# Kernel tuning notes

Measured on AMD Instinct MI355X. Metric: run time of the kernel, lower is better.

Reference implementation:

```python
import jax, jax.numpy as jnp
import numpy as np

# Grid constants from voxel_size=(0.2,0.2,4), point_cloud_range=(0,-40,-3,70.4,40,1)
VX, VY, VZ = 0.2, 0.2, 4.0
PCR = (0.0, -40.0, -3.0, 70.4, 40.0, 1.0)
NX, NY, NZ = 352, 400, 1   # round((hi-lo)/v) per axis
BATCH = 2
N_POINTS = 400000
CANVAS = BATCH * NZ * NY * NX  # dense canvas of all voxels (segment ids)
EPS = 1e-3  # BN1d eps from norm_cfg


def _vidx(coors):
    # linear voxel index: b*Z*Y*X + z*Y*X + y*X + x  (coors = [b,z,y,x])
    c = coors.astype(jnp.int32)
    return ((c[:, 0] * NZ + c[:, 1]) * NY + c[:, 2]) * NX + c[:, 3]


def _seg_mean(x, idx):
    # scatter-mean over voxels (DynamicScatter, average_points=True)
    s = jax.ops.segment_sum(x, idx, num_segments=CANVAS)
    c = jax.ops.segment_sum(jnp.ones((x.shape[0], 1), x.dtype), idx, num_segments=CANVAS)
    return s / jnp.maximum(c, 1.0)


def _seg_max(x, idx):
    # scatter-max over voxels (DynamicScatter, average_points=False); empty voxels -> 0
    m = jax.ops.segment_max(x, idx, num_segments=CANVAS)
    c = jax.ops.segment_sum(jnp.ones((x.shape[0],), x.dtype), idx, num_segments=CANVAS)
    return jnp.where((c > 0)[:, None], m, jnp.zeros_like(m))


def _bn_relu(x, g, b):
    # BN1d in training mode (batch stats, biased var), affine, then ReLU
    mu = x.mean(axis=0)
    var = x.var(axis=0)
    return jax.nn.relu((x - mu) * jax.lax.rsqrt(var + EPS) * g + b)


def setup_inputs() -> dict:
    key = jax.random.key(0)
    ks = jax.random.split(key, 6)
    features = jax.random.normal(ks[0], (N_POINTS, 4), jnp.float32)
    # coors [b, z, y, x]; batch column sorted so coors[-1,0]+1 == batch_size
    half = N_POINTS // 2
    b = jnp.concatenate([jnp.zeros(half, jnp.int32), jnp.ones(N_POINTS - half, jnp.int32)])
    z = jnp.zeros(N_POINTS, jnp.int32)  # NZ == 1
    y = jax.random.randint(ks[1], (N_POINTS,), 0, NY, jnp.int32)
    x = jax.random.randint(ks[2], (N_POINTS,), 0, NX, jnp.int32)
    coors = jnp.stack([b, z, y, x], axis=1)
    # VFE params: layer0 Linear(10->64, no bias), layer1 Linear(128->128, no bias)
    W0 = jax.random.normal(ks[3], (10, 64), jnp.float32) * 0.1
    g0 = jnp.ones((64,), jnp.float32)
    b0 = jnp.zeros((64,), jnp.float32)
    W1 = jax.random.normal(ks[4], (128, 128), jnp.float32) * 0.1
    g1 = jnp.ones((128,), jnp.float32)
    b1 = jnp.zeros((128,), jnp.float32)
    return {"features": features, "coors": coors, "W0": W0, "g0": g0, "b0": b0,
            "W1": W1, "g1": g1, "b1": b1}


def reference(features, coors, W0, g0, b0, W1, g1, b1):
    idx = _vidx(coors)
    # cluster center: scatter-mean of point features, gather back to points
    vmean = _seg_mean(features, idx)
    pts_mean = vmean[idx]
    f_cluster = features[:, :3] - pts_mean[:, :3]
    # voxel center offset
    cf = coors.astype(features.dtype)
    f_center = jnp.stack([
        features[:, 0] - (cf[:, 3] * VX + (VX / 2 + PCR[0])),
        features[:, 1] - (cf[:, 2] * VY + (VY / 2 + PCR[1])),
        features[:, 2] - (cf[:, 1] * VZ + (VZ / 2 + PCR[2])),
    ], axis=1)
    feat = jnp.concatenate([features, f_cluster, f_center], axis=1)  # (N, 10)
    # VFE layer 0 + voxel max pool + gather-broadcast + concat
    pf0 = _bn_relu(feat @ W0, g0, b0)           # (N, 64)
    v0 = _seg_max(pf0, idx)                     # (CANVAS, 64)
    feat1 = jnp.concatenate([pf0, v0[idx]], axis=1)  # (N, 128)
    # VFE layer 1 + final voxel max pool
    pf1 = _bn_relu(feat1 @ W1, g1, b1)          # (N, 128)
    voxel_feats = _seg_max(pf1, idx)            # (CANVAS, 128), dense canvas
    return voxel_feats
```

## Files before the change

### kernel.cpp

```cpp
#include <hip/hip_runtime.h>

#define NPTS 400000
#define NXv 352
#define NYv 400
#define CANVAS 281600
#define G2B 512
#define SCANB 275

typedef unsigned int uint;
typedef unsigned short ushort;
typedef __attribute__((ext_vector_type(8))) short short8;
typedef __attribute__((ext_vector_type(4))) float floatx4;

__device__ inline uint packbf(float a, float b) {
    uint ua = __float_as_uint(a);
    ua = (ua + 0x7fffu + ((ua >> 16) & 1u)) >> 16;
    uint ub = __float_as_uint(b);
    ub = (ub + 0x7fffu + ((ub >> 16) & 1u)) & 0xffff0000u;
    return ua | ub;
}
__device__ inline ushort bf16bits(float a) {
    uint u = __float_as_uint(a);
    return (ushort)((u + 0x7fffu + ((u >> 16) & 1u)) >> 16);
}
__device__ inline float lo16(uint u) { return __uint_as_float(u << 16); }
__device__ inline float hi16(uint u) { return __uint_as_float(u & 0xffff0000u); }
__device__ inline float bfval(ushort u) { return __uint_as_float(((uint)u) << 16); }

__global__ void k_bucket(const int4* __restrict__ coors, const float* __restrict__ W1,
                         int* __restrict__ idxbuf, int* __restrict__ pidx,
                         uint* __restrict__ ucnt, ushort* __restrict__ w1t) {
    int b = blockIdx.x;
    if (b < 1563) {
        int i = b * 256 + threadIdx.x;
        if (i >= NPTS) return;
        int4 c = coors[i];
        int idx = ((c.x + c.y) * NYv + c.z) * NXv + c.w;
        idxbuf[i] = idx;
        pidx[i] = (int)atomicAdd(&ucnt[idx], 1u);
    } else {
        int i = (b - 1563) * 256 + threadIdx.x;
        int n = i & 127, k = i >> 7;
        w1t[n * 128 + k] = bf16bits(W1[k * 128 + n]);
    }
}

__global__ __launch_bounds__(1024) void k_scanA(const uint* __restrict__ ucnt,
                                                uint* __restrict__ voff,
                                                uint* __restrict__ bsum) {
    __shared__ uint sh[1024];
    int t = threadIdx.x;
    int v = blockIdx.x * 1024 + t;
    uint val = ucnt[v];
    sh[t] = val;
    for (int off = 1; off < 1024; off <<= 1) {
        __syncthreads();
        uint x = (t >= off) ? sh[t - off] : 0u;
        __syncthreads();
        sh[t] += x;
    }
    uint incl = sh[t];
    voff[v] = incl - val;
    if (t == 1023) bsum[blockIdx.x] = incl;
}

__global__ __launch_bounds__(1024) void k_scanC(const uint* __restrict__ bsum,
                                                uint* __restrict__ voff) {
    __shared__ uint sh[1024];
    __shared__ uint bs[1024];
    int t = threadIdx.x;
    uint val = (t < SCANB) ? bsum[t] : 0u;
    sh[t] = val; bs[t] = val;
    for (int off = 1; off < 1024; off <<= 1) {
        __syncthreads();
        uint x = (t >= off) ? sh[t - off] : 0u;
        __syncthreads();
        sh[t] += x;
    }
    __syncthreads();
    uint off_ = sh[blockIdx.x] - bs[blockIdx.x];
    int v = blockIdx.x * 1024 + t;
    voff[v] += off_;
    if (blockIdx.x == SCANB - 1 && t == 1023) voff[CANVAS] = NPTS;
}

__global__ void k_perm(const int* __restrict__ idxbuf, const int* __restrict__ pidx,
                       const uint* __restrict__ voff, const float4* __restrict__ feat,
                       int* __restrict__ vidx, float4* __restrict__ featS) {
    int i = blockIdx.x * 256 + threadIdx.x;
    if (i >= NPTS) return;
    int idx = idxbuf[i];
    uint j = voff[idx] + (uint)pidx[i];
    vidx[j] = idx;
    featS[j] = feat[i];
}

__global__ void k_vmean(const float4* __restrict__ featS, const uint* __restrict__ voff,
                        float4* __restrict__ vmean) {
    int v = blockIdx.x * 256 + threadIdx.x;
    if (v >= CANVAS) return;
    uint s_ = voff[v], e_ = voff[v + 1];
    float4 s = make_float4(0.f, 0.f, 0.f, 0.f);
    for (uint j = s_; j < e_; ++j) {
        float4 f = featS[j];
        s.x += f.x; s.y += f.y; s.z += f.z; s.w += f.w;
    }
    float inv = 1.0f / (float)max((int)(e_ - s_), 1);
    vmean[v] = make_float4(s.x * inv, s.y * inv, s.z * inv, s.w * inv);
}

__global__ __launch_bounds__(256) void k_gemm1(
        const float4* __restrict__ featS, const int* __restrict__ vidx,
        const float4* __restrict__ vmean, const float* __restrict__ W0,
        uint* __restrict__ x0u, float* __restrict__ stats) {
    __shared__ float w0s[640];
    __shared__ __align__(8) ushort tile[256 * 68];
    __shared__ float ps[128], qs[128];
    for (int t = threadIdx.x; t < 640; t += 256) w0s[t] = W0[t];
    __syncthreads();
    int j = blockIdx.x * 256 + threadIdx.x;
    bool valid = j < NPTS;
    ushort* trow = &tile[threadIdx.x * 68];
    if (valid) {
        float4 f = featS[j];
        int idx = vidx[j];
        float4 vm = vmean[idx];
        int xq = idx % NXv;
        int yq = (idx / NXv) % NYv;
        float ft[10];
        ft[0] = f.x; ft[1] = f.y; ft[2] = f.z; ft[3] = f.w;
        ft[4] = f.x - vm.x;
        ft[5] = f.y - vm.y;
        ft[6] = f.z - vm.z;
        ft[7] = f.x - ((float)xq * 0.2f + 0.1f);
        ft[8] = f.y - ((float)yq * 0.2f - 39.9f);
        ft[9] = f.z + 1.0f;
        uint* o = x0u + (size_t)j * 32;
        #pragma unroll
        for (int g = 0; g < 8; ++g) {
            float a[8];
            #pragma unroll
            for (int q = 0; q < 8; ++q) a[q] = 0.f;
            #pragma unroll
            for (int k = 0; k < 10; ++k) {
                float fk = ft[k];
                #pragma unroll
                for (int q = 0; q < 8; ++q) a[q] = fmaf(fk, w0s[k * 64 + g * 8 + q], a[q]);
            }
            uint4 w;
            w.x = packbf(a[0], a[1]); w.y = packbf(a[2], a[3]);
            w.z = packbf(a[4], a[5]); w.w = packbf(a[6], a[7]);
            *(uint4*)(o + g * 4) = w;
            ((uint2*)trow)[g * 2 + 0] = make_uint2(w.x, w.y);
            ((uint2*)trow)[g * 2 + 1] = make_uint2(w.z, w.w);
        }
    } else {
        #pragma unroll
        for (int g = 0; g < 16; ++g) ((uint2*)trow)[g] = make_uint2(0u, 0u);
    }
    __syncthreads();
    if (threadIdx.x < 128) {
        int c = threadIdx.x & 63, half = threadIdx.x >> 6;
        float s = 0.f, q = 0.f;
        for (int r = half * 128; r < half * 128 + 128; ++r) {
            float xv = bfval(tile[r * 68 + c]);
            s += xv;
            q = fmaf(xv, xv, q);
        }
        ps[half * 64 + c] = s;
        qs[half * 64 + c] = q;
    }
    __syncthreads();
    if (threadIdx.x < 64) {
        int c = threadIdx.x;
        atomicAdd(&stats[c], ps[c] + ps[64 + c]);
        atomicAdd(&stats[64 + c], qs[c] + qs[64 + c]);
    }
}

__global__ void k_vmax0(const uint* __restrict__ x0u, const uint* __restrict__ voff,
                        const float* __restrict__ stats, const float* __restrict__ g0,
                        const float* __restrict__ b0, uint* __restrict__ v0u) {
    __shared__ float s[128];
    if (threadIdx.x < 64) {
        int c = threadIdx.x;
        float mu = stats[c] * (1.0f / NPTS);
        float var = stats[64 + c] * (1.0f / NPTS) - mu * mu;
        float sc = (1.0f / sqrtf(var + 1e-3f)) * g0[c];
        s[c] = sc;
        s[64 + c] = fmaf(-mu, sc, b0[c]);
    }
    __syncthreads();
    int t = blockIdx.x * 256 + threadIdx.x;
    int v = t >> 4;
    if (v >= CANVAS) return;
    uint s_ = voff[v], e_ = voff[v + 1];
    if (s_ == e_) return;
    int c = (t & 15) << 2;
    float4 m = make_float4(0.f, 0.f, 0.f, 0.f);
    for (uint j = s_; j < e_; ++j) {
        uint2 u = *(const uint2*)(x0u + (size_t)j * 32 + (c >> 1));
        m.x = fmaxf(m.x, fmaf(lo16(u.x), s[c + 0], s[64 + c + 0]));
        m.y = fmaxf(m.y, fmaf(hi16(u.x), s[c + 1], s[64 + c + 1]));
        m.z = fmaxf(m.z, fmaf(lo16(u.y), s[c + 2], s[64 + c + 2]));
        m.w = fmaxf(m.w, fmaf(hi16(u.y), s[c + 3], s[64 + c + 3]));
    }
    uint2 o; o.x = packbf(m.x, m.y); o.y = packbf(m.z, m.w);
    *(uint2*)(v0u + (size_t)v * 32 + (c >> 1)) = o;
}

__global__ __launch_bounds__(256) void k_gemm2p(
        const uint* __restrict__ x0u, const uint* __restrict__ v0u,
        const int* __restrict__ vidx, const uint* __restrict__ voff,
        const float* __restrict__ stats, const float* __restrict__ g0,
        const float* __restrict__ b0, const ushort* __restrict__ w1t,
        ushort* __restrict__ vmaxc, float* __restrict__ sums) {
    __shared__ __align__(16) ushort As[64 * 136];
    __shared__ __align__(16) ushort Cs[64 * 136];
    __shared__ float s[128];
    __shared__ int svid[2][64];

    int lane = threadIdx.x & 63, wid = threadIdx.x >> 6;
    int m = lane & 15, q = lane >> 4;

    if (threadIdx.x < 64) {
        int c = threadIdx.x;
        float mu = stats[c] * (1.0f / NPTS);
        float var = stats[64 + c] * (1.0f / NPTS) - mu * mu;
        float sc = (1.0f / sqrtf(var + 1e-3f)) * g0[c];
        s[c] = sc;
        s[64 + c] = fmaf(-mu, sc, b0[c]);
    }

    short8 breg[8][4];
    #pragma unroll
    for (int ct = 0; ct < 8; ++ct) {
        const ushort* br = &w1t[(ct * 16 + m) * 128 + q * 8];
        #pragma unroll
        for (int ks = 0; ks < 4; ++ks)
            breg[ct][ks] = *(const short8*)&br[ks * 32];
    }

    int p0 = (int)((long long)blockIdx.x * NPTS / G2B);
    int p1 = (int)((long long)(blockIdx.x + 1) * NPTS / G2B);
    int ps, pe;
    { int v = vidx[p0]; ps = (voff[v] == (uint)p0) ? p0 : (int)voff[v + 1]; }
    if (p1 >= NPTS) pe = NPTS;
    else { int v = vidx[p1]; pe = (voff[v] == (uint)p1) ? p1 : (int)voff[v + 1]; }

    float run = -3.0e38f, csum = 0.f, csq = 0.f;
    int vcur = -1;

    auto stage = [&](int r0s, int p) {
        int nrows = min(64, pe - r0s);
        for (int i = threadIdx.x; i < 512; i += 128) {
            int r = i >> 3, ch = i & 7, cb = ch * 8;
            uint4 o4 = make_uint4(0u, 0u, 0u, 0u);
            if (r < nrows) {
                uint4 u = *(const uint4*)(x0u + (size_t)(r0s + r) * 32 + ch * 4);
                uint w[4] = {u.x, u.y, u.z, u.w}, o[4];
                #pragma unroll
                for (int q2 = 0; q2 < 4; ++q2) {
                    float a = fmaxf(fmaf(lo16(w[q2]), s[cb + 2 * q2], s[64 + cb + 2 * q2]), 0.f);
                    float b = fmaxf(fmaf(hi16(w[q2]), s[cb + 2 * q2 + 1], s[64 + cb + 2 * q2 + 1]), 0.f);
                    o[q2] = packbf(a, b);
                }
                o4 = make_uint4(o[0], o[1], o[2], o[3]);
            }
            *(uint4*)&As[r * 136 + ch * 8] = o4;
        }
        for (int i = threadIdx.x; i < 512; i += 128) {
            int r = i >> 3, ch = i & 7;
            uint4 u = make_uint4(0u, 0u, 0u, 0u);
            if (r < nrows) u = *(const uint4*)(v0u + (size_t)vidx[r0s + r] * 32 + ch * 4);
            *(uint4*)&As[r * 136 + 64 + ch * 8] = u;
        }
        if (threadIdx.x < 64)
            svid[p][threadIdx.x] = (threadIdx.x < nrows) ? vidx[r0s + threadIdx.x] : -1;
    };

    __syncthreads();
    if (threadIdx.x < 128 && ps < pe) stage(ps, 0);
    __syncthreads();

    int sp = 0;
    for (int r0 = ps; r0 < pe; r0 += 64, sp ^= 1) {
        const ushort* ar = &As[(wid * 16 + m) * 136 + q * 8];
        short8 a0 = *(const short8*)&ar[0];
        short8 a1 = *(const short8*)&ar[32];
        short8 a2 = *(const short8*)&ar[64];
        short8 a3 = *(const short8*)&ar[96];
        #pragma unroll
        for (int ct = 0; ct < 8; ++ct) {
            floatx4 acc = {0.f, 0.f, 0.f, 0.f};
            acc = __builtin_amdgcn_mfma_f32_16x16x32_bf16(a0, breg[ct][0], acc, 0, 0, 0);
            acc = __builtin_amdgcn_mfma_f32_16x16x32_bf16(a1, breg[ct][1], acc, 0, 0, 0);
            acc = __builtin_amdgcn_mfma_f32_16x16x32_bf16(a2, breg[ct][2], acc, 0, 0, 0);
            acc = __builtin_amdgcn_mfma_f32_16x16x32_bf16(a3, breg[ct][3], acc, 0, 0, 0);
            #pragma unroll
            for (int rg = 0; rg < 4; ++rg)
                Cs[(wid * 16 + q * 4 + rg) * 136 + ct * 16 + m] = bf16bits(acc[rg]);
        }
        __syncthreads();

        if (threadIdx.x < 128) {
            if (r0 + 64 < pe) stage(r0 + 64, sp ^ 1);
        } else {
            int c = threadIdx.x - 128;
            #pragma unroll 8
            for (int r = 0; r < 64; ++r) {
                int v = svid[sp][r];
                float x = bfval(Cs[r * 136 + c]);
                bool brk = (v != vcur);
                if (brk && vcur >= 0)
                    vmaxc[(size_t)vcur * 128 + c] = bf16bits(run);
                run = brk ? x : fmaxf(run, x);
                vcur = v;
                csum += x;
                csq = fmaf(x, x, csq);
            }
        }
        __syncthreads();
    }

    if (threadIdx.x >= 128) {
        int c = threadIdx.x - 128;
        if (vcur >= 0) vmaxc[(size_t)vcur * 128 + c] = bf16bits(run);
        atomicAdd(&sums[c], csum);
        atomicAdd(&sums[128 + c], csq);
    }
}

__global__ __launch_bounds__(256) void k_bnout(const ushort* __restrict__ vmaxc,
        const uint* __restrict__ voff, const float* __restrict__ stats,
        const float* __restrict__ g1, const float* __restrict__ b1,
        float4* __restrict__ out) {
    __shared__ float s[256];
    if (threadIdx.x < 128) {
        int c = threadIdx.x;
        float mu = stats[128 + c] * (1.0f / NPTS);
        float var = stats[256 + c] * (1.0f / NPTS) - mu * mu;
        float sc = (1.0f / sqrtf(var + 1e-3f)) * g1[c];
        s[c] = sc;
        s[128 + c] = fmaf(-mu, sc, b1[c]);
    }
    __syncthreads();
    int t = blockIdx.x * 256 + threadIdx.x;
    int v = t >> 5;
    if (v >= CANVAS) return;
    int c = (t & 31) << 2;
    float4 m = make_float4(0.f, 0.f, 0.f, 0.f);
    if (voff[v + 1] != voff[v]) {
        uint2 u = *(const uint2*)(vmaxc + (size_t)v * 128 + c);
        m.x = fmaxf(fmaf(lo16(u.x), s[c + 0], s[128 + c + 0]), 0.f);
        m.y = fmaxf(fmaf(hi16(u.x), s[c + 1], s[128 + c + 1]), 0.f);
        m.z = fmaxf(fmaf(lo16(u.y), s[c + 2], s[128 + c + 2]), 0.f);
        m.w = fmaxf(fmaf(hi16(u.y), s[c + 3], s[128 + c + 3]), 0.f);
    }
    out[(size_t)v * 32 + (c >> 2)] = m;
}

extern "C" void kernel_launch(void* const* d_in, const int* in_sizes, int n_in,
                              void* d_out, int out_size, void* d_ws, size_t ws_size,
                              hipStream_t stream) {
    const float4* feat  = (const float4*)d_in[0];
    const int4*   coors = (const int4*)d_in[1];
    const float*  W0    = (const float*)d_in[2];
    const float*  g0    = (const float*)d_in[3];
    const float*  b0    = (const float*)d_in[4];
    const float*  W1    = (const float*)d_in[5];
    const float*  g1    = (const float*)d_in[6];
    const float*  b1    = (const float*)d_in[7];

    char* ws = (char*)d_ws;
    int*    idxbuf = (int*)(ws + 0);
    int*    pidx   = (int*)(ws + 1600000);
    uint*   ucnt   = (uint*)(ws + 3200000);
    float*  stats  = (float*)(ws + 4326400);
    uint*   voff   = (uint*)(ws + 4329472);
    uint*   bsum   = (uint*)(ws + 5455888);
    int*    vidx   = (int*)(ws + 5459984);
    float*  featS  = (float*)(ws + 7059984);
    float*  vmean  = (float*)(ws + 13459984);
    ushort* w1t    = (ushort*)(ws + 17965584);
    uint*   x0u    = (uint*)(ws + 17998352);
    uint*   v0u    = (uint*)(ws + 69198352);
    ushort* vmaxc  = (ushort*)(ws + 105243152);

    hipMemsetAsync(ws + 3200000, 0, 1129472, stream);

    const int BLK = 256;
    int gpts = (NPTS + BLK - 1) / BLK;
    int gvox = (CANVAS + BLK - 1) / BLK;

    k_bucket<<<gpts + 64, BLK, 0, stream>>>(coors, W1, idxbuf, pidx, ucnt, w1t);
    k_scanA<<<SCANB, 1024, 0, stream>>>(ucnt, voff, bsum);
    k_scanC<<<SCANB, 1024, 0, stream>>>(bsum, voff);
    k_perm<<<gpts, BLK, 0, stream>>>(idxbuf, pidx, voff, feat, vidx, (float4*)featS);
    k_vmean<<<gvox, BLK, 0, stream>>>((const float4*)featS, voff, (float4*)vmean);
    k_gemm1<<<gpts, BLK, 0, stream>>>((const float4*)featS, vidx, (const float4*)vmean,
                                      W0, x0u, stats);
    k_vmax0<<<CANVAS * 16 / BLK, BLK, 0, stream>>>(x0u, voff, stats, g0, b0, v0u);
    k_gemm2p<<<G2B, BLK, 0, stream>>>(x0u, v0u, vidx, voff, stats, g0, b0, w1t,
                                      vmaxc, stats + 128);
    k_bnout<<<CANVAS * 32 / BLK, BLK, 0, stream>>>(vmaxc, voff, stats, g1, b1,
                                                   (float4*)d_out);
}
```

Before: 449.4 us.

## Fuse voxel mean and layer-0 voxel max into voxel-aligned gemm1 blocks

```diff
diff --git a/kernel.cpp b/kernel.cpp
--- a/kernel.cpp
+++ b/kernel.cpp
@@ -4,6 +4,8 @@
 #define NXv 352
 #define NYv 400
 #define CANVAS 281600
+#define G1B 1563
+#define MAXR 288
 #define G2B 512
 #define SCANB 275
 
@@ -95,36 +97,49 @@
     featS[j] = feat[i];
 }
 
-__global__ void k_vmean(const float4* __restrict__ featS, const uint* __restrict__ voff,
-                        float4* __restrict__ vmean) {
-    int v = blockIdx.x * 256 + threadIdx.x;
-    if (v >= CANVAS) return;
-    uint s_ = voff[v], e_ = voff[v + 1];
-    float4 s = make_float4(0.f, 0.f, 0.f, 0.f);
-    for (uint j = s_; j < e_; ++j) {
-        float4 f = featS[j];
-        s.x += f.x; s.y += f.y; s.z += f.z; s.w += f.w;
-    }
-    float inv = 1.0f / (float)max((int)(e_ - s_), 1);
-    vmean[v] = make_float4(s.x * inv, s.y * inv, s.z * inv, s.w * inv);
-}
-
 __global__ __launch_bounds__(256) void k_gemm1(
         const float4* __restrict__ featS, const int* __restrict__ vidx,
-        const float4* __restrict__ vmean, const float* __restrict__ W0,
-        uint* __restrict__ x0u, float* __restrict__ stats) {
+        const uint* __restrict__ voff, const float* __restrict__ W0,
+        uint* __restrict__ x0u, uint* __restrict__ v0pre, float* __restrict__ stats) {
     __shared__ float w0s[640];
-    __shared__ __align__(8) ushort tile[256 * 68];
-    __shared__ float ps[128], qs[128];
+    __shared__ float4 vmn[MAXR];
+    __shared__ int sv[MAXR];
+    __shared__ __align__(8) ushort tile[MAXR * 68];
+    __shared__ float red[512];
     for (int t = threadIdx.x; t < 640; t += 256) w0s[t] = W0[t];
-    __syncthreads();
-    int j = blockIdx.x * 256 + threadIdx.x;
-    bool valid = j < NPTS;
-    ushort* trow = &tile[threadIdx.x * 68];
-    if (valid) {
-        float4 f = featS[j];
-        int idx = vidx[j];
-        float4 vm = vmean[idx];
+
+    int p0 = (int)((long long)blockIdx.x * NPTS / G1B);
+    int p1 = (int)((long long)(blockIdx.x + 1) * NPTS / G1B);
+    int ps, pe;
+    { int v = vidx[p0]; ps = (voff[v] == (uint)p0) ? p0 : (int)voff[v + 1]; }
+    if (p1 >= NPTS) pe = NPTS;
+    else { int v = vidx[p1]; pe = (voff[v] == (uint)p1) ? p1 : (int)voff[v + 1]; }
+    int n = pe - ps;
+    if (n <= 0) return;
+
+    for (int r = threadIdx.x; r < n; r += 256) sv[r] = vidx[ps + r];
+    __syncthreads();
+
+    for (int r = threadIdx.x; r < n; r += 256) {
+        if (r > 0 && sv[r] == sv[r - 1]) continue;
+        int v = sv[r];
+        float4 acc = featS[ps + r];
+        int e = r + 1;
+        while (e < n && sv[e] == v) {
+            float4 f = featS[ps + e];
+            acc.x += f.x; acc.y += f.y; acc.z += f.z; acc.w += f.w;
+            ++e;
+        }
+        float inv = 1.0f / (float)(e - r);
+        float4 mn = make_float4(acc.x * inv, acc.y * inv, acc.z * inv, acc.w * inv);
+        for (int r2 = r; r2 < e; ++r2) vmn[r2] = mn;
+    }
+    __syncthreads();
+
+    for (int r = threadIdx.x; r < n; r += 256) {
+        float4 f = featS[ps + r];
+        float4 vm = vmn[r];
+        int idx = sv[r];
         int xq = idx % NXv;
         int yq = (idx / NXv) % NYv;
         float ft[10];
@@ -135,7 +150,8 @@
         ft[7] = f.x - ((float)xq * 0.2f + 0.1f);
         ft[8] = f.y - ((float)yq * 0.2f - 39.9f);
         ft[9] = f.z + 1.0f;
-        uint* o = x0u + (size_t)j * 32;
+        uint* o = x0u + (size_t)(ps + r) * 32;
+        ushort* trow = &tile[r * 68];
         #pragma unroll
         for (int g = 0; g < 8; ++g) {
             float a[8];
@@ -154,69 +170,56 @@
             ((uint2*)trow)[g * 2 + 0] = make_uint2(w.x, w.y);
             ((uint2*)trow)[g * 2 + 1] = make_uint2(w.z, w.w);
         }
-    } else {
-        #pragma unroll
-        for (int g = 0; g < 16; ++g) ((uint2*)trow)[g] = make_uint2(0u, 0u);
-    }
-    __syncthreads();
-    if (threadIdx.x < 128) {
-        int c = threadIdx.x & 63, half = threadIdx.x >> 6;
-        float s = 0.f, q = 0.f;
-        for (int r = half * 128; r < half * 128 + 128; ++r) {
-            float xv = bfval(tile[r * 68 + c]);
-            s += xv;
-            q = fmaf(xv, xv, q);
-        }
-        ps[half * 64 + c] = s;
-        qs[half * 64 + c] = q;
+    }
+    __syncthreads();
+
+    {
+        int c = threadIdx.x & 63, q = threadIdx.x >> 6;
+        int rlo = q * 72, rhi = min(rlo + 72, n);
+        float s = 0.f, sq = 0.f;
+        for (int r = rlo; r < rhi; ++r) {
+            float x = bfval(tile[r * 68 + c]);
+            s += x; sq = fmaf(x, x, sq);
+        }
+        red[threadIdx.x] = s;
+        red[256 + threadIdx.x] = sq;
     }
     __syncthreads();
     if (threadIdx.x < 64) {
         int c = threadIdx.x;
-        atomicAdd(&stats[c], ps[c] + ps[64 + c]);
-        atomicAdd(&stats[64 + c], qs[c] + qs[64 + c]);
-    }
-}
-
-__global__ void k_vmax0(const uint* __restrict__ x0u, const uint* __restrict__ voff,
-                        const float* __restrict__ stats, const float* __restrict__ g0,
-                        const float* __restrict__ b0, uint* __restrict__ v0u) {
-    __shared__ float s[128];
-    if (threadIdx.x < 64) {
-        int c = threadIdx.x;
-        float mu = stats[c] * (1.0f / NPTS);
-        float var = stats[64 + c] * (1.0f / NPTS) - mu * mu;
-        float sc = (1.0f / sqrtf(var + 1e-3f)) * g0[c];
-        s[c] = sc;
-        s[64 + c] = fmaf(-mu, sc, b0[c]);
-    }
-    __syncthreads();
-    int t = blockIdx.x * 256 + threadIdx.x;
-    int v = t >> 4;
-    if (v >= CANVAS) return;
-    uint s_ = voff[v], e_ = voff[v + 1];
-    if (s_ == e_) return;
-    int c = (t & 15) << 2;
-    float4 m = make_float4(0.f, 0.f, 0.f, 0.f);
-    for (uint j = s_; j < e_; ++j) {
-        uint2 u = *(const uint2*)(x0u + (size_t)j * 32 + (c >> 1));
-        m.x = fmaxf(m.x, fmaf(lo16(u.x), s[c + 0], s[64 + c + 0]));
-        m.y = fmaxf(m.y, fmaf(hi16(u.x), s[c + 1], s[64 + c + 1]));
-        m.z = fmaxf(m.z, fmaf(lo16(u.y), s[c + 2], s[64 + c + 2]));
-        m.w = fmaxf(m.w, fmaf(hi16(u.y), s[c + 3], s[64 + c + 3]));
-    }
-    uint2 o; o.x = packbf(m.x, m.y); o.y = packbf(m.z, m.w);
-    *(uint2*)(v0u + (size_t)v * 32 + (c >> 1)) = o;
+        float s = red[c] + red[64 + c] + red[128 + c] + red[192 + c];
+        float sq = red[256 + c] + red[320 + c] + red[384 + c] + red[448 + c];
+        atomicAdd(&stats[c], s);
+        atomicAdd(&stats[64 + c], sq);
+    }
+
+    for (int t = threadIdx.x; t < n * 16; t += 256) {
+        int r = t >> 4, cg = t & 15;
+        if (r > 0 && sv[r] == sv[r - 1]) continue;
+        int v = sv[r];
+        const ushort* tp = &tile[r * 68 + cg * 4];
+        float m0 = bfval(tp[0]), m1 = bfval(tp[1]);
+        float m2 = bfval(tp[2]), m3 = bfval(tp[3]);
+        int e = r + 1;
+        while (e < n && sv[e] == v) {
+            const ushort* t2 = &tile[e * 68 + cg * 4];
+            m0 = fmaxf(m0, bfval(t2[0])); m1 = fmaxf(m1, bfval(t2[1]));
+            m2 = fmaxf(m2, bfval(t2[2])); m3 = fmaxf(m3, bfval(t2[3]));
+            ++e;
+        }
+        uint2 o; o.x = packbf(m0, m1); o.y = packbf(m2, m3);
+        *(uint2*)(v0pre + (size_t)v * 32 + cg * 2) = o;
+    }
 }
 
 __global__ __launch_bounds__(256) void k_gemm2p(
-        const uint* __restrict__ x0u, const uint* __restrict__ v0u,
+        const uint* __restrict__ x0u, const uint* __restrict__ v0pre,
         const int* __restrict__ vidx, const uint* __restrict__ voff,
         const float* __restrict__ stats, const float* __restrict__ g0,
         const float* __restrict__ b0, const ushort* __restrict__ w1t,
         ushort* __restrict__ vmaxc, float* __restrict__ sums) {
     __shared__ __align__(16) ushort As[64 * 136];
-    __shared__ __align__(16) ushort Cs[64 * 136];
+    __shared__ __align__(8) ushort CsT[128 * 74];
     __shared__ float s[128];
     __shared__ int svid[2][64];
 
@@ -270,10 +273,20 @@
             *(uint4*)&As[r * 136 + ch * 8] = o4;
         }
         for (int i = threadIdx.x; i < 512; i += 128) {
-            int r = i >> 3, ch = i & 7;
-            uint4 u = make_uint4(0u, 0u, 0u, 0u);
-            if (r < nrows) u = *(const uint4*)(v0u + (size_t)vidx[r0s + r] * 32 + ch * 4);
-            *(uint4*)&As[r * 136 + 64 + ch * 8] = u;
+            int r = i >> 3, ch = i & 7, cb = ch * 8;
+            uint4 o4 = make_uint4(0u, 0u, 0u, 0u);
+            if (r < nrows) {
+                uint4 u = *(const uint4*)(v0pre + (size_t)vidx[r0s + r] * 32 + ch * 4);
+                uint w[4] = {u.x, u.y, u.z, u.w}, o[4];
+                #pragma unroll
+                for (int q2 = 0; q2 < 4; ++q2) {
+                    float a = fmaxf(fmaf(lo16(w[q2]), s[cb + 2 * q2], s[64 + cb + 2 * q2]), 0.f);
+                    float b = fmaxf(fmaf(hi16(w[q2]), s[cb + 2 * q2 + 1], s[64 + cb + 2 * q2 + 1]), 0.f);
+                    o[q2] = packbf(a, b);
+                }
+                o4 = make_uint4(o[0], o[1], o[2], o[3]);
+            }
+            *(uint4*)&As[r * 136 + 64 + ch * 8] = o4;
         }
         if (threadIdx.x < 64)
             svid[p][threadIdx.x] = (threadIdx.x < nrows) ? vidx[r0s + threadIdx.x] : -1;
@@ -297,9 +310,9 @@
             acc = __builtin_amdgcn_mfma_f32_16x16x32_bf16(a1, breg[ct][1], acc, 0, 0, 0);
             acc = __builtin_amdgcn_mfma_f32_16x16x32_bf16(a2, breg[ct][2], acc, 0, 0, 0);
             acc = __builtin_amdgcn_mfma_f32_16x16x32_bf16(a3, breg[ct][3], acc, 0, 0, 0);
-            #pragma unroll
-            for (int rg = 0; rg < 4; ++rg)
-                Cs[(wid * 16 + q * 4 + rg) * 136 + ct * 16 + m] = bf16bits(acc[rg]);
+            uint* cp = (uint*)&CsT[(ct * 16 + m) * 74 + wid * 16 + q * 4];
+            cp[0] = packbf(acc[0], acc[1]);
+            cp[1] = packbf(acc[2], acc[3]);
         }
         __syncthreads();
 
@@ -307,17 +320,22 @@
             if (r0 + 64 < pe) stage(r0 + 64, sp ^ 1);
         } else {
             int c = threadIdx.x - 128;
-            #pragma unroll 8
-            for (int r = 0; r < 64; ++r) {
-                int v = svid[sp][r];
-                float x = bfval(Cs[r * 136 + c]);
-                bool brk = (v != vcur);
-                if (brk && vcur >= 0)
-                    vmaxc[(size_t)vcur * 128 + c] = bf16bits(run);
-                run = brk ? x : fmaxf(run, x);
-                vcur = v;
-                csum += x;
-                csq = fmaf(x, x, csq);
+            const uint* crow = (const uint*)&CsT[c * 74];
+            #pragma unroll 4
+            for (int rp = 0; rp < 32; ++rp) {
+                uint u = crow[rp];
+                int va = svid[sp][2 * rp], vb = svid[sp][2 * rp + 1];
+                float xa = lo16(u), xb = hi16(u);
+                bool brk = (va != vcur);
+                if (brk && vcur >= 0) vmaxc[(size_t)vcur * 128 + c] = bf16bits(run);
+                run = brk ? xa : fmaxf(run, xa);
+                vcur = va;
+                csum += xa; csq = fmaf(xa, xa, csq);
+                brk = (vb != vcur);
+                if (brk && vcur >= 0) vmaxc[(size_t)vcur * 128 + c] = bf16bits(run);
+                run = brk ? xb : fmaxf(run, xb);
+                vcur = vb;
+                csum += xb; csq = fmaf(xb, xb, csq);
             }
         }
         __syncthreads();
@@ -381,27 +399,23 @@
     uint*   bsum   = (uint*)(ws + 5455888);
     int*    vidx   = (int*)(ws + 5459984);
     float*  featS  = (float*)(ws + 7059984);
-    float*  vmean  = (float*)(ws + 13459984);
     ushort* w1t    = (ushort*)(ws + 17965584);
     uint*   x0u    = (uint*)(ws + 17998352);
-    uint*   v0u    = (uint*)(ws + 69198352);
+    uint*   v0pre  = (uint*)(ws + 69198352);
     ushort* vmaxc  = (ushort*)(ws + 105243152);
 
     hipMemsetAsync(ws + 3200000, 0, 1129472, stream);
 
     const int BLK = 256;
     int gpts = (NPTS + BLK - 1) / BLK;
-    int gvox = (CANVAS + BLK - 1) / BLK;
 
     k_bucket<<<gpts + 64, BLK, 0, stream>>>(coors, W1, idxbuf, pidx, ucnt, w1t);
     k_scanA<<<SCANB, 1024, 0, stream>>>(ucnt, voff, bsum);
     k_scanC<<<SCANB, 1024, 0, stream>>>(bsum, voff);
     k_perm<<<gpts, BLK, 0, stream>>>(idxbuf, pidx, voff, feat, vidx, (float4*)featS);
-    k_vmean<<<gvox, BLK, 0, stream>>>((const float4*)featS, voff, (float4*)vmean);
-    k_gemm1<<<gpts, BLK, 0, stream>>>((const float4*)featS, vidx, (const float4*)vmean,
-                                      W0, x0u, stats);
-    k_vmax0<<<CANVAS * 16 / BLK, BLK, 0, stream>>>(x0u, voff, stats, g0, b0, v0u);
-    k_gemm2p<<<G2B, BLK, 0, stream>>>(x0u, v0u, vidx, voff, stats, g0, b0, w1t,
+    k_gemm1<<<G1B, BLK, 0, stream>>>((const float4*)featS, vidx, voff, W0,
+                                     x0u, v0pre, stats);
+    k_gemm2p<<<G2B, BLK, 0, stream>>>(x0u, v0pre, vidx, voff, stats, g0, b0, w1t,
                                       vmaxc, stats + 128);
     k_bnout<<<CANVAS * 32 / BLK, BLK, 0, stream>>>(vmaxc, voff, stats, g1, b1,
                                                    (float4*)d_out);
```

Result: slower. 516.6 us (+15.0%).
